# Performance work log

Hardware: AMD Instinct MI355X
Metric: run time of the kernel (lower is better)

Reference implementation:

```python
import jax, jax.numpy as jnp
import numpy as np
import math

# B queries, N complex ambient dim, M codebook entries, S payload dim, K quad nodes
B, N, M, S, K = 1024, 128, 8192, 256, 8
EPS_TOTAL = 1e-3
OVERLAP, ANISO = 0.25, 0.75
_t, _w = np.polynomial.hermite.hermgauss(K)
GH_T = jnp.asarray(_t, jnp.float32)
GH_W = jnp.asarray(_w, jnp.float32)


def _init_sigmas():
    # mirrors CPSFFusedCodebook._init_sigmas (log-space for numerical safety at N=128)
    rho = 1.0 + ANISO
    logV = (N / 2.0) * math.log(math.pi) - math.lgamma(N / 2.0 + 1.0)
    log_r = (math.log(OVERLAP) - math.log(M) - logV - math.log(rho)) / N
    r_perp = math.exp(log_r)
    s_perp = 2.0 * math.pi * r_perp ** 2
    return rho * rho * s_perp, s_perp


def setup_inputs() -> dict:
    key = jax.random.key(0)
    ks = jax.random.split(key, 12)
    u = lambda k, sh: jax.random.uniform(k, sh, jnp.float32, -1.0, 1.0)
    s_par, s_perp = _init_sigmas()
    return {
        "z_re": u(ks[0], (B, N)), "z_im": u(ks[1], (B, N)),
        "d_re": u(ks[2], (B, N)), "d_im": u(ks[3], (B, N)),
        "zj_re": 0.5 * u(ks[4], (M, N)), "zj_im": 0.5 * u(ks[5], (M, N)),
        "dj_re": 0.5 * u(ks[6], (M, N)), "dj_im": 0.5 * u(ks[7], (M, N)),
        "T_re": u(ks[8], (M, S)), "T_im": u(ks[9], (M, S)),
        "alpha": jax.random.uniform(ks[10], (M,), jnp.float32, 0.5, 1.5),
        "sigma_par": jnp.full((M,), s_par, jnp.float32),
        "sigma_perp": jnp.full((M,), s_perp, jnp.float32),
    }


def _unit(xr, xi):
    n = jnp.sqrt(jnp.sum(xr * xr + xi * xi, -1, keepdims=True))
    n = jnp.where(n == 0, jnp.ones_like(n), n)
    return xr / n, xi / n


def _forward(z_re, z_im, d_re, d_im, zj_re, zj_im, dj_re, dj_im,
             T_re, T_im, alpha, sigma_par, sigma_perp):
    tiny = jnp.float32(np.finfo(np.float32).tiny)
    dur, dui = _unit(d_re, d_im)          # autonorm_vec_d
    djr, dji = _unit(dj_re, dj_im)        # autonorm_vec_d_j
    a = jnp.maximum(alpha, tiny)
    sp = jnp.maximum(sigma_par, tiny)
    sq = jnp.maximum(sigma_perp, tiny)

    # proj[b,m] = <d_j, z - z_j> (conj-linear in d_j); all via GEMMs, no [B,M,N] tensor
    pr = z_re @ djr.T + z_im @ dji.T - jnp.sum(djr * zj_re + dji * zj_im, -1)[None, :]
    pi = z_im @ djr.T - z_re @ dji.T - jnp.sum(djr * zj_im - dji * zj_re, -1)[None, :]

    # |z - z_j|^2 via GEMM expansion
    dz2 = (jnp.sum(z_re * z_re + z_im * z_im, -1)[:, None]
           + jnp.sum(zj_re * zj_re + zj_im * zj_im, -1)[None, :]
           - 2.0 * (z_re @ zj_re.T + z_im @ zj_im.T))
    perp2 = jnp.maximum(dz2 - (pr * pr + pi * pi), 0.0)  # component orthogonal to d_j

    # Gauss-Hermite quadrature along the codebook direction, scaled per-code
    scale = jnp.sqrt(sp / jnp.pi)                     # [M]
    t = GH_T[None, :] * scale[:, None]                # [M,K] quad offsets
    par2 = (pr[:, :, None] - t[None]) ** 2 + (pi * pi)[:, :, None]   # [B,M,K]
    env = jnp.exp(-jnp.pi * (par2 / sp[None, :, None]
                             + (perp2 / sq[None, :])[:, :, None]))
    rho = jnp.einsum('bmk,k->bm', env, GH_W) * (scale / jnp.sqrt(jnp.pi))[None, :]

    # angular alignment |<d_j, d>|^2
    ar = dur @ djr.T + dui @ dji.T
    ai = dui @ djr.T - dur @ dji.T
    align = ar * ar + ai * ai

    w = a[None, :] * align * rho                      # [B,M] real mixture weights
    den = jnp.sum(w, -1) + EPS_TOTAL                  # [B]
    out_re = (w @ T_re) / den[:, None]                # [B,S]
    out_im = (w @ T_im) / den[:, None]
    return jnp.stack([out_re, out_im], -1)            # [B,S,2] == complex [B,S]


def reference(z_re, z_im, d_re, d_im, zj_re, zj_im, dj_re, dj_im,
              T_re, T_im, alpha, sigma_par, sigma_perp):
    return _forward(z_re, z_im, d_re, d_im, zj_re, zj_im, dj_re, dj_im,
                    T_re, T_im, alpha, sigma_par, sigma_perp)
```

## Files before the change

### kernel.cpp

```cpp
#include <hip/hip_runtime.h>
#include <math.h>

#define Bq 1024
#define Nn 128
#define Mm 8192
#define Ss 256

typedef _Float16 f16;
typedef _Float16 f16x8 __attribute__((ext_vector_type(8)));
typedef _Float16 f16x4 __attribute__((ext_vector_type(4)));
typedef float f32x4 __attribute__((ext_vector_type(4)));

#define PI_F 3.14159265358979323846f
#define INV_SQRT_PI 0.5641895835477563f
#define TINY_F 1.17549435e-38f
#define EPS_TOTAL 1e-3f
#define WSC 1024.0f

#define GLOAD16(g, l) \
    __builtin_amdgcn_global_load_lds((const __attribute__((address_space(1))) void*)(g), \
                                     (__attribute__((address_space(3))) void*)(l), 16, 0, 0)

__global__ void cpsf_prep_b(const float* __restrict__ z_re, const float* __restrict__ z_im,
                            const float* __restrict__ d_re, const float* __restrict__ d_im,
                            float* __restrict__ z2, float* __restrict__ invd)
{
    const int b = blockIdx.x * 4 + (threadIdx.x >> 6);
    const int l = threadIdx.x & 63;
    const int o = b * Nn;
    float dr0 = d_re[o + l], dr1 = d_re[o + l + 64];
    float di0 = d_im[o + l], di1 = d_im[o + l + 64];
    float zr0 = z_re[o + l], zr1 = z_re[o + l + 64];
    float zi0 = z_im[o + l], zi1 = z_im[o + l + 64];
    float sd = dr0*dr0 + di0*di0 + dr1*dr1 + di1*di1;
    float sz = zr0*zr0 + zi0*zi0 + zr1*zr1 + zi1*zi1;
#pragma unroll
    for (int off = 1; off < 64; off <<= 1) {
        sd += __shfl_xor(sd, off);
        sz += __shfl_xor(sz, off);
    }
    if (l == 0) {
        float nd = sqrtf(sd);
        nd = (nd == 0.0f) ? 1.0f : nd;
        z2[b] = sz;
        invd[b] = 1.0f / nd;
    }
}

__global__ void cpsf_prep_m(const float* __restrict__ zj_re, const float* __restrict__ zj_im,
                            const float* __restrict__ dj_re, const float* __restrict__ dj_im,
                            const float* __restrict__ alpha, const float* __restrict__ sp_,
                            const float* __restrict__ sq_, float* __restrict__ cm)
{
    const int m = blockIdx.x * 4 + (threadIdx.x >> 6);
    const int l = threadIdx.x & 63;
    const int o = m * Nn;
    float dr0 = dj_re[o + l], dr1 = dj_re[o + l + 64];
    float di0 = dj_im[o + l], di1 = dj_im[o + l + 64];
    float zr0 = zj_re[o + l], zr1 = zj_re[o + l + 64];
    float zi0 = zj_im[o + l], zi1 = zj_im[o + l + 64];
    float snd = dr0*dr0 + di0*di0 + dr1*dr1 + di1*di1;
    float sc1 = dr0*zr0 + di0*zi0 + dr1*zr1 + di1*zi1;
    float sc2 = dr0*zi0 - di0*zr0 + dr1*zi1 - di1*zr1;
    float sz2 = zr0*zr0 + zi0*zi0 + zr1*zr1 + zi1*zi1;
#pragma unroll
    for (int off = 1; off < 64; off <<= 1) {
        snd += __shfl_xor(snd, off);
        sc1 += __shfl_xor(sc1, off);
        sc2 += __shfl_xor(sc2, off);
        sz2 += __shfl_xor(sz2, off);
    }
    if (l == 0) {
        float nd = sqrtf(snd);
        nd = (nd == 0.0f) ? 1.0f : nd;
        float inv = 1.0f / nd;
        cm[0*Mm + m] = inv;
        cm[1*Mm + m] = sc1 * inv;
        cm[2*Mm + m] = sc2 * inv;
        cm[3*Mm + m] = sz2;
        float sp = fmaxf(sp_[m], TINY_F);
        float sq = fmaxf(sq_[m], TINY_F);
        float sc = sqrtf(sp / PI_F);
        cm[4*Mm + m] = PI_F / sp;
        cm[5*Mm + m] = PI_F / sq;
        cm[6*Mm + m] = fmaxf(alpha[m], TINY_F) * sc * INV_SQRT_PI;
        cm[7*Mm + m] = sc;
    }
}

__global__ void cpsf_pack_ab(const float* __restrict__ z_re, const float* __restrict__ z_im,
                             const float* __restrict__ d_re, const float* __restrict__ d_im,
                             const float* __restrict__ invd, f16* __restrict__ Az, f16* __restrict__ Au)
{
    int idx = blockIdx.x * 256 + threadIdx.x;
    int b = idx >> 6, k4 = (idx & 63) * 4;
    float4 vz, vd;
    if (k4 < 128) {
        vz = *(const float4*)(z_re + b * Nn + k4);
        vd = *(const float4*)(d_re + b * Nn + k4);
    } else {
        vz = *(const float4*)(z_im + b * Nn + k4 - 128);
        vd = *(const float4*)(d_im + b * Nn + k4 - 128);
    }
    float s = invd[b];
    *(f16x4*)(Az + b * 256 + k4) = (f16x4){(f16)vz.x, (f16)vz.y, (f16)vz.z, (f16)vz.w};
    *(f16x4*)(Au + b * 256 + k4) = (f16x4){(f16)(vd.x*s), (f16)(vd.y*s), (f16)(vd.z*s), (f16)(vd.w*s)};
}

__global__ void cpsf_pack_b1(const float* __restrict__ zj_re, const float* __restrict__ zj_im,
                             const float* __restrict__ dj_re, const float* __restrict__ dj_im,
                             const float* __restrict__ cm, f16* __restrict__ Bp,
                             int Mc, int m0g, int mshift)
{
    int idx = blockIdx.x * 256 + threadIdx.x;
    int r = idx >> 6, k4 = (idx & 63) * 4;
    int p = r >> mshift, ml = r & (Mc - 1);
    int m = m0g + ml;
    float4 v; float s;
    if (p == 0) {
        v = (k4 < 128) ? *(const float4*)(dj_re + m * Nn + k4)
                       : *(const float4*)(dj_im + m * Nn + k4 - 128);
        s = cm[m];
    } else if (p == 1) {
        if (k4 < 128) { v = *(const float4*)(dj_im + m * Nn + k4); v.x=-v.x; v.y=-v.y; v.z=-v.z; v.w=-v.w; }
        else          { v = *(const float4*)(dj_re + m * Nn + k4 - 128); }
        s = cm[m];
    } else {
        v = (k4 < 128) ? *(const float4*)(zj_re + m * Nn + k4)
                       : *(const float4*)(zj_im + m * Nn + k4 - 128);
        s = 1.0f;
    }
    *(f16x4*)(Bp + (size_t)r * 256 + k4) = (f16x4){(f16)(v.x*s), (f16)(v.y*s), (f16)(v.z*s), (f16)(v.w*s)};
}

__global__ void cpsf_pack_tt(const float* __restrict__ T_re, const float* __restrict__ T_im,
                             f16* __restrict__ Tt, int Mc, int m0g)
{
    __shared__ float tr[64][65], ti[64][65];
    const int mb = blockIdx.x * 64, sb = blockIdx.y * 64;
    const int tid = threadIdx.x;
    const int i0 = tid >> 6, j = tid & 63;
#pragma unroll
    for (int it = 0; it < 16; ++it) {
        int i = it * 4 + i0;
        tr[i][j] = T_re[(size_t)(m0g + mb + i) * Ss + sb + j];
        ti[i][j] = T_im[(size_t)(m0g + mb + i) * Ss + sb + j];
    }
    __syncthreads();
#pragma unroll
    for (int it = 0; it < 16; ++it) {
        int jj = it * 4 + i0;
        int sp = (sb + jj) * 2;
        Tt[(size_t)sp * Mc + mb + j]       = (f16)tr[j][jj];
        Tt[(size_t)(sp + 1) * Mc + mb + j] = (f16)ti[j][jj];
    }
}

__global__ __launch_bounds__(256, 2) void cpsf_gemm_w(
    const f16* __restrict__ Az, const f16* __restrict__ Au,
    const f16* __restrict__ Bp, const float* __restrict__ cm,
    const float* __restrict__ z2v, f16* __restrict__ wbuf,
    float* __restrict__ den, int Mc, int m0g)
{
    __shared__ __align__(16) f16 sm[2 * 1792 * 8];

    const int tid = threadIdx.x;
    const int wid = tid >> 6;
    const int lane = tid & 63;
    const int q = lane >> 4;
    const int li = lane & 15;
    const int mb0 = blockIdx.x * 64;
    const int bb0 = blockIdx.y * 128;
    const int wb0 = (wid >> 1) * 64;
    const int wm0 = (wid & 1) * 32;
    const int BUFO = 1792 * 8;

    const f16* gp[7];
    f16* lb[7];
#pragma unroll
    for (int i = 0; i < 7; ++i) {
        int c = i * 4 + wid;
        const f16* src;
        if (c < 8) {
            int g = c >> 1, row = (c & 1) * 64 + lane;
            src = Az + (size_t)(bb0 + row) * 256 + g * 8;
        } else if (c < 16) {
            int c2 = c - 8;
            int g = c2 >> 1, row = (c2 & 1) * 64 + lane;
            src = Au + (size_t)(bb0 + row) * 256 + g * 8;
        } else {
            int c2 = c - 16;
            int g = c2 / 3, p = c2 % 3;
            src = Bp + ((size_t)p * Mc + mb0 + lane) * 256 + g * 8;
        }
        gp[i] = src;
        lb[i] = sm + (size_t)(i * 256 + wid * 64) * 8;
    }

    f32x4 accP[4][2][3];
    f32x4 accQ[4][2][2];
#pragma unroll
    for (int t = 0; t < 4; ++t)
#pragma unroll
        for (int u = 0; u < 2; ++u) {
#pragma unroll
            for (int p = 0; p < 3; ++p) accP[t][u][p] = (f32x4){0.f,0.f,0.f,0.f};
#pragma unroll
            for (int p = 0; p < 2; ++p) accQ[t][u][p] = (f32x4){0.f,0.f,0.f,0.f};
        }

#pragma unroll
    for (int i = 0; i < 7; ++i) {
        GLOAD16(gp[i], lb[i]);
        gp[i] += 32;
    }
    __syncthreads();

#pragma unroll 2
    for (int ks = 0; ks < 8; ++ks) {
        const int buf = ks & 1;
        if (ks < 7) {
#pragma unroll
            for (int i = 0; i < 7; ++i) {
                GLOAD16(gp[i], lb[i] + (buf ^ 1) * BUFO);
                gp[i] += 32;
            }
        }

        const f16* bs = sm + buf * BUFO;
        f16x8 az[4], au[4], bf[3][2];
#pragma unroll
        for (int t = 0; t < 4; ++t) {
            az[t] = *(const f16x8*)(bs + (size_t)(q * 128 + wb0 + t * 16 + li) * 8);
            au[t] = *(const f16x8*)(bs + (size_t)(512 + q * 128 + wb0 + t * 16 + li) * 8);
        }
#pragma unroll
        for (int p = 0; p < 3; ++p)
#pragma unroll
            for (int u = 0; u < 2; ++u)
                bf[p][u] = *(const f16x8*)(bs + (size_t)(1024 + q * 192 + p * 64 + wm0 + u * 16 + li) * 8);

#pragma unroll
        for (int t = 0; t < 4; ++t)
#pragma unroll
            for (int u = 0; u < 2; ++u) {
#pragma unroll
                for (int p = 0; p < 3; ++p)
                    accP[t][u][p] = __builtin_amdgcn_mfma_f32_16x16x32_f16(az[t], bf[p][u], accP[t][u][p], 0, 0, 0);
#pragma unroll
                for (int p = 0; p < 2; ++p)
                    accQ[t][u][p] = __builtin_amdgcn_mfma_f32_16x16x32_f16(au[t], bf[p][u], accQ[t][u][p], 0, 0, 0);
            }

        __syncthreads();
    }

    const float GT[8] = {-2.9306374202572440f, -1.9816567566958429f,
                         -1.1571937124467802f, -0.3811869902073221f,
                          0.3811869902073221f,  1.1571937124467802f,
                          1.9816567566958429f,  2.9306374202572440f};
    const float GW[8] = {1.9960407221136762e-04f, 1.7077983007413475e-02f,
                         2.0780232581489188e-01f, 6.6114701255824129e-01f,
                         6.6114701255824129e-01f, 2.0780232581489188e-01f,
                         1.7077983007413475e-02f, 1.9960407221136762e-04f};

    float c1[2], c2[2], zj2[2], isp[2], isq[2], cf[2], scl[2];
#pragma unroll
    for (int u = 0; u < 2; ++u) {
        int mg = m0g + mb0 + wm0 + u * 16 + li;
        c1[u]  = cm[1*Mm + mg];  c2[u]  = cm[2*Mm + mg];
        zj2[u] = cm[3*Mm + mg];  isp[u] = cm[4*Mm + mg];
        isq[u] = cm[5*Mm + mg];  cf[u]  = cm[6*Mm + mg];
        scl[u] = cm[7*Mm + mg];
    }

    float dsum[4][4];
#pragma unroll
    for (int t = 0; t < 4; ++t)
#pragma unroll
        for (int r = 0; r < 4; ++r) dsum[t][r] = 0.f;

#pragma unroll
    for (int t = 0; t < 4; ++t) {
#pragma unroll
        for (int r = 0; r < 4; ++r) {
            const int b = bb0 + wb0 + t * 16 + q * 4 + r;
            const float z2b = z2v[b];
#pragma unroll
            for (int u = 0; u < 2; ++u) {
                float pr = accP[t][u][0][r] - c1[u];
                float pi = accP[t][u][1][r] - c2[u];
                float dz2 = z2b + zj2[u] - 2.0f * accP[t][u][2][r];
                float perp2 = fmaxf(dz2 - pr * pr - pi * pi, 0.0f);
                float base = -(isq[u] * perp2 + isp[u] * pi * pi);
                float rho = 0.0f;
#pragma unroll
                for (int k = 0; k < 8; ++k) {
                    float dd = pr - scl[u] * GT[k];
                    rho = fmaf(GW[k], __expf(base - isp[u] * dd * dd), rho);
                }
                float ar = accQ[t][u][0][r], ai = accQ[t][u][1][r];
                float wv = cf[u] * (ar * ar + ai * ai) * rho;
                dsum[t][r] += wv;
                wbuf[(size_t)b * Mc + mb0 + wm0 + u * 16 + li] = (f16)(wv * WSC);
            }
        }
    }
#pragma unroll
    for (int t = 0; t < 4; ++t)
#pragma unroll
        for (int r = 0; r < 4; ++r) {
            float v = dsum[t][r];
            v += __shfl_xor(v, 1);
            v += __shfl_xor(v, 2);
            v += __shfl_xor(v, 4);
            v += __shfl_xor(v, 8);
            if (li == 0) atomicAdd(den + bb0 + wb0 + t * 16 + q * 4 + r, v);
        }
}

__global__ __launch_bounds__(256, 3) void cpsf_gemm_out(
    const f16* __restrict__ wbuf, const f16* __restrict__ Tt,
    float* __restrict__ oacc, int Mc, int Kw)
{
    __shared__ __align__(16) f16 sm[2 * 1024 * 8];
    const int tid = threadIdx.x;
    const int wid = tid >> 6;
    const int lane = tid & 63;
    const int q = lane >> 4;
    const int li = lane & 15;
    const int sb0 = blockIdx.x * 128;
    const int bb0 = blockIdx.y * 128;
    const int kz0 = blockIdx.z * Kw;
    const int wb0 = (wid >> 1) * 64;
    const int ws0 = (wid & 1) * 64;
    const int BUFO = 1024 * 8;

    const f16* gp[4];
    f16* lb[4];
#pragma unroll
    for (int i = 0; i < 4; ++i) {
        int c = i * 4 + wid;
        const f16* src;
        if (c < 8) {
            int g = c >> 1, row = (c & 1) * 64 + lane;
            src = wbuf + (size_t)(bb0 + row) * Mc + kz0 + g * 8;
        } else {
            int c2 = c - 8;
            int g = c2 >> 1, row = (c2 & 1) * 64 + lane;
            src = Tt + (size_t)(sb0 + row) * Mc + kz0 + g * 8;
        }
        gp[i] = src;
        lb[i] = sm + (size_t)(i * 256 + wid * 64) * 8;
    }

    f32x4 acc[4][4];
#pragma unroll
    for (int t = 0; t < 4; ++t)
#pragma unroll
        for (int u = 0; u < 4; ++u) acc[t][u] = (f32x4){0.f,0.f,0.f,0.f};

#pragma unroll
    for (int i = 0; i < 4; ++i) {
        GLOAD16(gp[i], lb[i]);
        gp[i] += 32;
    }
    __syncthreads();

    const int nk = Kw >> 5;
    for (int kc = 0; kc < nk; ++kc) {
        const int buf = kc & 1;
        if (kc + 1 < nk) {
#pragma unroll
            for (int i = 0; i < 4; ++i) {
                GLOAD16(gp[i], lb[i] + (buf ^ 1) * BUFO);
                gp[i] += 32;
            }
        }
        const f16* bs = sm + buf * BUFO;
        f16x8 af[4], bf[4];
#pragma unroll
        for (int t = 0; t < 4; ++t)
            af[t] = *(const f16x8*)(bs + (size_t)(q * 128 + wb0 + t * 16 + li) * 8);
#pragma unroll
        for (int u = 0; u < 4; ++u)
            bf[u] = *(const f16x8*)(bs + (size_t)(512 + q * 128 + ws0 + u * 16 + li) * 8);
#pragma unroll
        for (int t = 0; t < 4; ++t)
#pragma unroll
            for (int u = 0; u < 4; ++u)
                acc[t][u] = __builtin_amdgcn_mfma_f32_16x16x32_f16(af[t], bf[u], acc[t][u], 0, 0, 0);
        __syncthreads();
    }
#pragma unroll
    for (int t = 0; t < 4; ++t)
#pragma unroll
        for (int u = 0; u < 4; ++u)
#pragma unroll
            for (int r = 0; r < 4; ++r)
                atomicAdd(oacc + (size_t)(bb0 + wb0 + t * 16 + q * 4 + r) * 512 + sb0 + ws0 + u * 16 + li,
                          acc[t][u][r]);
}

__global__ void cpsf_fin(const float* __restrict__ oacc, const float* __restrict__ den,
                         float* __restrict__ out)
{
    int i = blockIdx.x * 256 + threadIdx.x;
    float d = (den[i >> 9] + EPS_TOTAL) * WSC;
    out[i] = oacc[i] / d;
}

extern "C" void kernel_launch(void* const* d_in, const int* in_sizes, int n_in,
                              void* d_out, int out_size, void* d_ws, size_t ws_size,
                              hipStream_t stream)
{
    (void)in_sizes; (void)n_in; (void)out_size;
    const float* z_re  = (const float*)d_in[0];
    const float* z_im  = (const float*)d_in[1];
    const float* d_re  = (const float*)d_in[2];
    const float* d_im  = (const float*)d_in[3];
    const float* zj_re = (const float*)d_in[4];
    const float* zj_im = (const float*)d_in[5];
    const float* dj_re = (const float*)d_in[6];
    const float* dj_im = (const float*)d_in[7];
    const float* T_re  = (const float*)d_in[8];
    const float* T_im  = (const float*)d_in[9];
    const float* alpha = (const float*)d_in[10];
    const float* s_par = (const float*)d_in[11];
    const float* s_perp= (const float*)d_in[12];

    char* w8 = (char*)d_ws;
    const size_t o_out  = 0;
    const size_t o_den  = o_out + (size_t)Bq * 512 * 4;
    const size_t o_z2   = o_den + 4096;
    const size_t o_invd = o_z2 + 4096;
    const size_t o_cm   = o_invd + 4096;
    const size_t o_az   = o_cm + (size_t)8 * Mm * 4;
    const size_t o_au   = o_az + (size_t)Bq * 256 * 2;
    const size_t o_ch   = o_au + (size_t)Bq * 256 * 2;
    int Mc = 512;
    if      (o_ch + (size_t)4608 * 8192 <= ws_size) Mc = 8192;
    else if (o_ch + (size_t)4608 * 4096 <= ws_size) Mc = 4096;
    else if (o_ch + (size_t)4608 * 2048 <= ws_size) Mc = 2048;
    else if (o_ch + (size_t)4608 * 1024 <= ws_size) Mc = 1024;
    int mshift = 31 - __builtin_clz((unsigned)Mc);
    int zs = Mc / 512; if (zs < 1) zs = 1;
    int Kw = Mc / zs;

    float* oacc = (float*)(w8 + o_out);
    float* den  = (float*)(w8 + o_den);
    float* z2   = (float*)(w8 + o_z2);
    float* invd = (float*)(w8 + o_invd);
    float* cm   = (float*)(w8 + o_cm);
    f16*   Az   = (f16*)(w8 + o_az);
    f16*   Au   = (f16*)(w8 + o_au);
    f16*   Bp   = (f16*)(w8 + o_ch);
    f16*   Tt   = (f16*)(w8 + o_ch + (size_t)1536 * Mc);
    f16*   wb   = (f16*)(w8 + o_ch + (size_t)2560 * Mc);

    hipMemsetAsync(d_ws, 0, o_z2, stream);

    cpsf_prep_b<<<Bq / 4, 256, 0, stream>>>(z_re, z_im, d_re, d_im, z2, invd);
    cpsf_prep_m<<<Mm / 4, 256, 0, stream>>>(zj_re, zj_im, dj_re, dj_im, alpha, s_par, s_perp, cm);
    cpsf_pack_ab<<<(Bq * 64) / 256, 256, 0, stream>>>(z_re, z_im, d_re, d_im, invd, Az, Au);

    for (int m0 = 0; m0 < Mm; m0 += Mc) {
        cpsf_pack_b1<<<(3 * Mc * 64) / 256, 256, 0, stream>>>(zj_re, zj_im, dj_re, dj_im,
                                                              cm, Bp, Mc, m0, mshift);
        cpsf_pack_tt<<<dim3(Mc / 64, Ss / 64), 256, 0, stream>>>(T_re, T_im, Tt, Mc, m0);
        cpsf_gemm_w<<<dim3(Mc / 64, Bq / 128), 256, 0, stream>>>(Az, Au, Bp, cm, z2, wb, den, Mc, m0);
        cpsf_gemm_out<<<dim3(4, Bq / 128, zs), 256, 0, stream>>>(wb, Tt, oacc, Mc, Kw);
    }
    cpsf_fin<<<(Bq * 512) / 256, 256, 0, stream>>>(oacc, den, (float*)d_out);
}
```

Before: 246.5 us.

## Pre-swizzle GEMM operands into MFMA fragment layout and load directly to registers

The pack kernels now write A and B operands in a k-chunk-major layout that matches the MFMA fragment order, so cpsf_gemm_w reads fragments straight from global memory into registers with software double-buffering. This drops the LDS staging, the async global-to-LDS copies and the per-step barriers. The 1/|d_j| normalization moves out of the packed B operand and into the epilogue as a multiply on the accumulators. The risks are that register-direct global loads rely on L2/L1 reuse across waves instead of shared LDS, and that unnormalized d_j values in fp16 change rounding slightly.

```diff
diff --git a/kernel.cpp b/kernel.cpp
--- a/kernel.cpp
+++ b/kernel.cpp
@@ -90,47 +90,44 @@
 
 __global__ void cpsf_pack_ab(const float* __restrict__ z_re, const float* __restrict__ z_im,
                              const float* __restrict__ d_re, const float* __restrict__ d_im,
-                             const float* __restrict__ invd, f16* __restrict__ Az, f16* __restrict__ Au)
+                             const float* __restrict__ invd, f16* __restrict__ Az)
 {
     int idx = blockIdx.x * 256 + threadIdx.x;
-    int b = idx >> 6, k4 = (idx & 63) * 4;
-    float4 vz, vd;
-    if (k4 < 128) {
-        vz = *(const float4*)(z_re + b * Nn + k4);
-        vd = *(const float4*)(d_re + b * Nn + k4);
-    } else {
-        vz = *(const float4*)(z_im + b * Nn + k4 - 128);
-        vd = *(const float4*)(d_im + b * Nn + k4 - 128);
-    }
-    float s = invd[b];
-    *(f16x4*)(Az + b * 256 + k4) = (f16x4){(f16)vz.x, (f16)vz.y, (f16)vz.z, (f16)vz.w};
-    *(f16x4*)(Au + b * 256 + k4) = (f16x4){(f16)(vd.x*s), (f16)(vd.y*s), (f16)(vd.z*s), (f16)(vd.w*s)};
+    int b = idx & 1023, mc = idx >> 10;
+    int map = mc >> 5, c = mc & 31;
+    int k8 = (c & 15) * 8;
+    const float* src;
+    float s;
+    if (map == 0) { src = (c < 16) ? z_re : z_im; s = 1.0f; }
+    else          { src = (c < 16) ? d_re : d_im; s = invd[b]; }
+    float4 v0 = *(const float4*)(src + (size_t)b * Nn + k8);
+    float4 v1 = *(const float4*)(src + (size_t)b * Nn + k8 + 4);
+    f16x8 o = {(f16)(v0.x*s), (f16)(v0.y*s), (f16)(v0.z*s), (f16)(v0.w*s),
+               (f16)(v1.x*s), (f16)(v1.y*s), (f16)(v1.z*s), (f16)(v1.w*s)};
+    *(f16x8*)(Az + (size_t)idx * 8) = o;
 }
 
 __global__ void cpsf_pack_b1(const float* __restrict__ zj_re, const float* __restrict__ zj_im,
                              const float* __restrict__ dj_re, const float* __restrict__ dj_im,
-                             const float* __restrict__ cm, f16* __restrict__ Bp,
-                             int Mc, int m0g, int mshift)
+                             f16* __restrict__ Bp, int Mc, int m0g, int mshift)
 {
     int idx = blockIdx.x * 256 + threadIdx.x;
-    int r = idx >> 6, k4 = (idx & 63) * 4;
-    int p = r >> mshift, ml = r & (Mc - 1);
-    int m = m0g + ml;
-    float4 v; float s;
-    if (p == 0) {
-        v = (k4 < 128) ? *(const float4*)(dj_re + m * Nn + k4)
-                       : *(const float4*)(dj_im + m * Nn + k4 - 128);
-        s = cm[m];
-    } else if (p == 1) {
-        if (k4 < 128) { v = *(const float4*)(dj_im + m * Nn + k4); v.x=-v.x; v.y=-v.y; v.z=-v.z; v.w=-v.w; }
-        else          { v = *(const float4*)(dj_re + m * Nn + k4 - 128); }
-        s = cm[m];
-    } else {
-        v = (k4 < 128) ? *(const float4*)(zj_re + m * Nn + k4)
-                       : *(const float4*)(zj_im + m * Nn + k4 - 128);
-        s = 1.0f;
-    }
-    *(f16x4*)(Bp + (size_t)r * 256 + k4) = (f16x4){(f16)(v.x*s), (f16)(v.y*s), (f16)(v.z*s), (f16)(v.w*s)};
+    int m = idx & (Mc - 1);
+    int pc = idx >> mshift;
+    int p = pc >> 5, c = pc & 31;
+    int mg = m0g + m;
+    int hi = (c >= 16);
+    int k8 = (c & 15) * 8;
+    const float* src;
+    float sgn = 1.0f;
+    if (p == 0)      src = hi ? dj_im : dj_re;
+    else if (p == 1) { src = hi ? dj_re : dj_im; sgn = hi ? 1.0f : -1.0f; }
+    else             src = hi ? zj_im : zj_re;
+    float4 v0 = *(const float4*)(src + (size_t)mg * Nn + k8);
+    float4 v1 = *(const float4*)(src + (size_t)mg * Nn + k8 + 4);
+    f16x8 o = {(f16)(v0.x*sgn), (f16)(v0.y*sgn), (f16)(v0.z*sgn), (f16)(v0.w*sgn),
+               (f16)(v1.x*sgn), (f16)(v1.y*sgn), (f16)(v1.z*sgn), (f16)(v1.w*sgn)};
+    *(f16x8*)(Bp + (size_t)idx * 8) = o;
 }
 
 __global__ void cpsf_pack_tt(const float* __restrict__ T_re, const float* __restrict__ T_im,
@@ -157,13 +154,10 @@
 }
 
 __global__ __launch_bounds__(256, 2) void cpsf_gemm_w(
-    const f16* __restrict__ Az, const f16* __restrict__ Au,
-    const f16* __restrict__ Bp, const float* __restrict__ cm,
-    const float* __restrict__ z2v, f16* __restrict__ wbuf,
-    float* __restrict__ den, int Mc, int m0g)
-{
-    __shared__ __align__(16) f16 sm[2 * 1792 * 8];
-
+    const f16* __restrict__ Az, const f16* __restrict__ Bp,
+    const float* __restrict__ cm, const float* __restrict__ z2v,
+    f16* __restrict__ wbuf, float* __restrict__ den, int Mc, int m0g)
+{
     const int tid = threadIdx.x;
     const int wid = tid >> 6;
     const int lane = tid & 63;
@@ -173,29 +167,14 @@
     const int bb0 = blockIdx.y * 128;
     const int wb0 = (wid >> 1) * 64;
     const int wm0 = (wid & 1) * 32;
-    const int BUFO = 1792 * 8;
-
-    const f16* gp[7];
-    f16* lb[7];
-#pragma unroll
-    for (int i = 0; i < 7; ++i) {
-        int c = i * 4 + wid;
-        const f16* src;
-        if (c < 8) {
-            int g = c >> 1, row = (c & 1) * 64 + lane;
-            src = Az + (size_t)(bb0 + row) * 256 + g * 8;
-        } else if (c < 16) {
-            int c2 = c - 8;
-            int g = c2 >> 1, row = (c2 & 1) * 64 + lane;
-            src = Au + (size_t)(bb0 + row) * 256 + g * 8;
-        } else {
-            int c2 = c - 16;
-            int g = c2 / 3, p = c2 % 3;
-            src = Bp + ((size_t)p * Mc + mb0 + lane) * 256 + g * 8;
-        }
-        gp[i] = src;
-        lb[i] = sm + (size_t)(i * 256 + wid * 64) * 8;
-    }
+
+    const f16* pAz = Az + ((size_t)(q) * 1024 + bb0 + wb0 + li) * 8;
+    const f16* pAu = pAz + (size_t)32 * 1024 * 8;
+    const f16* pB0 = Bp + ((size_t)(0 * 32 + q) * Mc + mb0 + wm0 + li) * 8;
+    const f16* pB1 = Bp + ((size_t)(1 * 32 + q) * Mc + mb0 + wm0 + li) * 8;
+    const f16* pB2 = Bp + ((size_t)(2 * 32 + q) * Mc + mb0 + wm0 + li) * 8;
+    const size_t KSA = (size_t)4 * 1024 * 8;
+    const size_t KSB = (size_t)4 * Mc * 8;
 
     f32x4 accP[4][2][3];
     f32x4 accQ[4][2][2];
@@ -209,51 +188,43 @@
             for (int p = 0; p < 2; ++p) accQ[t][u][p] = (f32x4){0.f,0.f,0.f,0.f};
         }
 
-#pragma unroll
-    for (int i = 0; i < 7; ++i) {
-        GLOAD16(gp[i], lb[i]);
-        gp[i] += 32;
-    }
-    __syncthreads();
-
-#pragma unroll 2
-    for (int ks = 0; ks < 8; ++ks) {
-        const int buf = ks & 1;
-        if (ks < 7) {
-#pragma unroll
-            for (int i = 0; i < 7; ++i) {
-                GLOAD16(gp[i], lb[i] + (buf ^ 1) * BUFO);
-                gp[i] += 32;
-            }
-        }
-
-        const f16* bs = sm + buf * BUFO;
-        f16x8 az[4], au[4], bf[3][2];
-#pragma unroll
-        for (int t = 0; t < 4; ++t) {
-            az[t] = *(const f16x8*)(bs + (size_t)(q * 128 + wb0 + t * 16 + li) * 8);
-            au[t] = *(const f16x8*)(bs + (size_t)(512 + q * 128 + wb0 + t * 16 + li) * 8);
-        }
-#pragma unroll
-        for (int p = 0; p < 3; ++p)
-#pragma unroll
-            for (int u = 0; u < 2; ++u)
-                bf[p][u] = *(const f16x8*)(bs + (size_t)(1024 + q * 192 + p * 64 + wm0 + u * 16 + li) * 8);
-
-#pragma unroll
-        for (int t = 0; t < 4; ++t)
-#pragma unroll
-            for (int u = 0; u < 2; ++u) {
-#pragma unroll
-                for (int p = 0; p < 3; ++p)
-                    accP[t][u][p] = __builtin_amdgcn_mfma_f32_16x16x32_f16(az[t], bf[p][u], accP[t][u][p], 0, 0, 0);
-#pragma unroll
-                for (int p = 0; p < 2; ++p)
-                    accQ[t][u][p] = __builtin_amdgcn_mfma_f32_16x16x32_f16(au[t], bf[p][u], accQ[t][u][p], 0, 0, 0);
-            }
-
-        __syncthreads();
-    }
+    f16x8 azA[4], auA[4], bfA[6], azB[4], auB[4], bfB[6];
+
+#define LOADSET(AZ, AU, BF, KS) do {                                              \
+    const size_t oA = (size_t)(KS) * KSA;                                         \
+    const size_t oB = (size_t)(KS) * KSB;                                         \
+    AZ[0] = *(const f16x8*)(pAz + oA);        AZ[1] = *(const f16x8*)(pAz + oA + 128); \
+    AZ[2] = *(const f16x8*)(pAz + oA + 256);  AZ[3] = *(const f16x8*)(pAz + oA + 384); \
+    AU[0] = *(const f16x8*)(pAu + oA);        AU[1] = *(const f16x8*)(pAu + oA + 128); \
+    AU[2] = *(const f16x8*)(pAu + oA + 256);  AU[3] = *(const f16x8*)(pAu + oA + 384); \
+    BF[0] = *(const f16x8*)(pB0 + oB);        BF[1] = *(const f16x8*)(pB0 + oB + 128); \
+    BF[2] = *(const f16x8*)(pB1 + oB);        BF[3] = *(const f16x8*)(pB1 + oB + 128); \
+    BF[4] = *(const f16x8*)(pB2 + oB);        BF[5] = *(const f16x8*)(pB2 + oB + 128); \
+} while (0)
+
+#define MFMASET(AZ, AU, BF) do {                                                  \
+    _Pragma("unroll")                                                             \
+    for (int t = 0; t < 4; ++t)                                                   \
+        _Pragma("unroll")                                                         \
+        for (int u = 0; u < 2; ++u) {                                             \
+            accP[t][u][0] = __builtin_amdgcn_mfma_f32_16x16x32_f16(AZ[t], BF[0*2+u], accP[t][u][0], 0, 0, 0); \
+            accP[t][u][1] = __builtin_amdgcn_mfma_f32_16x16x32_f16(AZ[t], BF[1*2+u], accP[t][u][1], 0, 0, 0); \
+            accP[t][u][2] = __builtin_amdgcn_mfma_f32_16x16x32_f16(AZ[t], BF[2*2+u], accP[t][u][2], 0, 0, 0); \
+            accQ[t][u][0] = __builtin_amdgcn_mfma_f32_16x16x32_f16(AU[t], BF[0*2+u], accQ[t][u][0], 0, 0, 0); \
+            accQ[t][u][1] = __builtin_amdgcn_mfma_f32_16x16x32_f16(AU[t], BF[1*2+u], accQ[t][u][1], 0, 0, 0); \
+        }                                                                         \
+} while (0)
+
+    LOADSET(azA, auA, bfA, 0);
+#pragma unroll
+    for (int kk = 0; kk < 4; ++kk) {
+        LOADSET(azB, auB, bfB, kk * 2 + 1);
+        MFMASET(azA, auA, bfA);
+        if (kk < 3) LOADSET(azA, auA, bfA, kk * 2 + 2);
+        MFMASET(azB, auB, bfB);
+    }
+#undef LOADSET
+#undef MFMASET
 
     const float GT[8] = {-2.9306374202572440f, -1.9816567566958429f,
                          -1.1571937124467802f, -0.3811869902073221f,
@@ -264,10 +235,11 @@
                          6.6114701255824129e-01f, 2.0780232581489188e-01f,
                          1.7077983007413475e-02f, 1.9960407221136762e-04f};
 
-    float c1[2], c2[2], zj2[2], isp[2], isq[2], cf[2], scl[2];
+    float iv[2], c1[2], c2[2], zj2[2], isp[2], isq[2], cf[2], scl[2];
 #pragma unroll
     for (int u = 0; u < 2; ++u) {
         int mg = m0g + mb0 + wm0 + u * 16 + li;
+        iv[u]  = cm[0*Mm + mg];
         c1[u]  = cm[1*Mm + mg];  c2[u]  = cm[2*Mm + mg];
         zj2[u] = cm[3*Mm + mg];  isp[u] = cm[4*Mm + mg];
         isq[u] = cm[5*Mm + mg];  cf[u]  = cm[6*Mm + mg];
@@ -288,8 +260,8 @@
             const float z2b = z2v[b];
 #pragma unroll
             for (int u = 0; u < 2; ++u) {
-                float pr = accP[t][u][0][r] - c1[u];
-                float pi = accP[t][u][1][r] - c2[u];
+                float pr = accP[t][u][0][r] * iv[u] - c1[u];
+                float pi = accP[t][u][1][r] * iv[u] - c2[u];
                 float dz2 = z2b + zj2[u] - 2.0f * accP[t][u][2][r];
                 float perp2 = fmaxf(dz2 - pr * pr - pi * pi, 0.0f);
                 float base = -(isq[u] * perp2 + isp[u] * pi * pi);
@@ -299,7 +271,7 @@
                     float dd = pr - scl[u] * GT[k];
                     rho = fmaf(GW[k], __expf(base - isp[u] * dd * dd), rho);
                 }
-                float ar = accQ[t][u][0][r], ai = accQ[t][u][1][r];
+                float ar = accQ[t][u][0][r] * iv[u], ai = accQ[t][u][1][r] * iv[u];
                 float wv = cf[u] * (ar * ar + ai * ai) * rho;
                 dsum[t][r] += wv;
                 wbuf[(size_t)b * Mc + mb0 + wm0 + u * 16 + li] = (f16)(wv * WSC);
@@ -436,8 +408,7 @@
     const size_t o_invd = o_z2 + 4096;
     const size_t o_cm   = o_invd + 4096;
     const size_t o_az   = o_cm + (size_t)8 * Mm * 4;
-    const size_t o_au   = o_az + (size_t)Bq * 256 * 2;
-    const size_t o_ch   = o_au + (size_t)Bq * 256 * 2;
+    const size_t o_ch   = o_az + (size_t)Bq * 512 * 2;
     int Mc = 512;
     if      (o_ch + (size_t)4608 * 8192 <= ws_size) Mc = 8192;
     else if (o_ch + (size_t)4608 * 4096 <= ws_size) Mc = 4096;
@@ -453,7 +424,6 @@
     float* invd = (float*)(w8 + o_invd);
     float* cm   = (float*)(w8 + o_cm);
     f16*   Az   = (f16*)(w8 + o_az);
-    f16*   Au   = (f16*)(w8 + o_au);
     f16*   Bp   = (f16*)(w8 + o_ch);
     f16*   Tt   = (f16*)(w8 + o_ch + (size_t)1536 * Mc);
     f16*   wb   = (f16*)(w8 + o_ch + (size_t)2560 * Mc);
@@ -462,13 +432,13 @@
 
     cpsf_prep_b<<<Bq / 4, 256, 0, stream>>>(z_re, z_im, d_re, d_im, z2, invd);
     cpsf_prep_m<<<Mm / 4, 256, 0, stream>>>(zj_re, zj_im, dj_re, dj_im, alpha, s_par, s_perp, cm);
-    cpsf_pack_ab<<<(Bq * 64) / 256, 256, 0, stream>>>(z_re, z_im, d_re, d_im, invd, Az, Au);
+    cpsf_pack_ab<<<(64 * 1024) / 256, 256, 0, stream>>>(z_re, z_im, d_re, d_im, invd, Az);
 
     for (int m0 = 0; m0 < Mm; m0 += Mc) {
-        cpsf_pack_b1<<<(3 * Mc * 64) / 256, 256, 0, stream>>>(zj_re, zj_im, dj_re, dj_im,
-                                                              cm, Bp, Mc, m0, mshift);
+        cpsf_pack_b1<<<(96 * Mc) / 256, 256, 0, stream>>>(zj_re, zj_im, dj_re, dj_im,
+                                                          Bp, Mc, m0, mshift);
         cpsf_pack_tt<<<dim3(Mc / 64, Ss / 64), 256, 0, stream>>>(T_re, T_im, Tt, Mc, m0);
-        cpsf_gemm_w<<<dim3(Mc / 64, Bq / 128), 256, 0, stream>>>(Az, Au, Bp, cm, z2, wb, den, Mc, m0);
+        cpsf_gemm_w<<<dim3(Mc / 64, Bq / 128), 256, 0, stream>>>(Az, Bp, cm, z2, wb, den, Mc, m0);
         cpsf_gemm_out<<<dim3(4, Bq / 128, zs), 256, 0, stream>>>(wb, Tt, oacc, Mc, Kw);
     }
     cpsf_fin<<<(Bq * 512) / 256, 256, 0, stream>>>(oacc, den, (float*)d_out);
```

Result: slower. 268.4 us (+8.9%).
